# Performance work log

Measured on AMD Instinct MI355X. Metric: run time of the kernel, lower is better.

The kernel has to match this reference:

```python
import jax, jax.numpy as jnp
import numpy as np

B, T, U, H, M, K, C = 64, 800, 80, 512, 20, 10, 80  # batch, tsteps, char len, rnn_size, nmixtures, kmixtures, char_vec_len


def _lstm(x, W, Uw, b):
    """Keras-semantics LSTM (gate order i,f,g,o), zero initial state. x: [B,T,D] -> [B,T,H]."""
    xg = jnp.einsum('btd,dh->bth', x, W) + b  # precompute input contribution
    h0 = jnp.zeros((x.shape[0], Uw.shape[0]), x.dtype)
    c0 = jnp.zeros_like(h0)

    def step(carry, zt):
        h, c = carry
        z = zt + h @ Uw
        i, f, g, o = jnp.split(z, 4, axis=-1)
        c = jax.nn.sigmoid(f) * c + jax.nn.sigmoid(i) * jnp.tanh(g)
        h = jax.nn.sigmoid(o) * jnp.tanh(c)
        return (h, c), h

    _, hs = jax.lax.scan(step, (h0, c0), jnp.swapaxes(xg, 0, 1))
    return jnp.swapaxes(hs, 0, 1)


def _forward(stroke_data, char_seq, kappa0, W0, U0, b0, W1, U1, b1, W2, U2, b2, Wa, ba, Wm, bm):
    lstm0_out = _lstm(stroke_data, W0, U0, b0)  # [B,T,H]
    # Attention window: the per-timestep loop in the source only carries kappa,
    # which is a running sum of exp(kappa_offset) -> vectorize via cumsum.
    abk = jnp.exp(jnp.einsum('bth,hk->btk', lstm0_out, Wa) + ba)  # [B,T,3K]
    alpha, beta, koff = jnpp_split = jnp.split(abk, 3, axis=-1)
    kappa = kappa0[:, None, :, 0] + jnp.cumsum(koff, axis=1)  # [B,T,K]
    u = jnp.arange(char_seq.shape[1], dtype=stroke_data.dtype)  # [U]
    # phi: [B,T,U] = sum_k alpha * exp(-beta * (kappa - u)^2)
    phi = jnp.sum(alpha[..., None] * jnp.exp(-beta[..., None] * (kappa[..., None] - u) ** 2), axis=2)
    windows = jnp.einsum('btu,buc->btc', phi, char_seq)  # [B,T,C]
    aug = jnp.concatenate([lstm0_out, windows, stroke_data], axis=-1)
    lstm1_out = _lstm(aug, W1, U1, b1)
    lstm2_out = _lstm(lstm1_out, W2, U2, b2)
    mdn = jnp.einsum('bth,hn->btn', lstm2_out, Wm) + bm  # [B,T,1+6M]
    eos_hat = mdn[..., 0:1]
    pi_hat, mu1, mu2, s1_hat, s2_hat, rho_hat = jnp.split(mdn[..., 1:], 6, axis=-1)
    return jnp.concatenate([
        jax.nn.sigmoid(-eos_hat),
        jax.nn.softmax(pi_hat, axis=-1),
        mu1, mu2,
        jnp.exp(s1_hat), jnp.exp(s2_hat),
        jnp.tanh(rho_hat),
    ], axis=-1)  # [B,T,1+6M]


def setup_inputs() -> dict:
    key = jax.random.key(0)
    ks = jax.random.split(key, 12)
    init = lambda k, shape: jax.random.truncated_normal(k, -2.0, 2.0, shape, jnp.float32) * 0.075
    return {
        'stroke_data': jax.random.normal(ks[0], (B, T, 3), jnp.float32),
        'char_seq': jax.nn.one_hot(jax.random.randint(ks[1], (B, U), 0, C), C, dtype=jnp.float32),
        'kappa0': jnp.zeros((B, K, 1), jnp.float32),
        'W0': init(ks[2], (3, 4 * H)), 'U0': init(ks[3], (H, 4 * H)), 'b0': jnp.zeros((4 * H,)),
        'W1': init(ks[4], (H + C + 3, 4 * H)), 'U1': init(ks[5], (H, 4 * H)), 'b1': jnp.zeros((4 * H,)),
        'W2': init(ks[6], (H, 4 * H)), 'U2': init(ks[7], (H, 4 * H)), 'b2': jnp.zeros((4 * H,)),
        'Wa': init(ks[8], (H, 3 * K)),
        'ba': -3.0 + 0.25 * jax.random.truncated_normal(ks[9], -2.0, 2.0, (3 * K,), jnp.float32),
        'Wm': init(ks[10], (H, 1 + 6 * M)), 'bm': jnp.zeros((1 + 6 * M,)),
    }


def reference(stroke_data, char_seq, kappa0, W0, U0, b0, W1, U1, b1, W2, U2, b2, Wa, ba, Wm, bm):
    return _forward(stroke_data, char_seq, kappa0, W0, U0, b0, W1, U1, b1, W2, U2, b2, Wa, ba, Wm, bm)
```

## Files before the change

kernel.cpp:

```cpp
#include <hip/hip_runtime.h>

typedef unsigned short u16;
typedef unsigned int u32;
typedef short v8s __attribute__((ext_vector_type(8)));
typedef float v4f __attribute__((ext_vector_type(4)));
typedef unsigned int v4u __attribute__((ext_vector_type(4)));
typedef unsigned int v2u __attribute__((ext_vector_type(2)));

#define MFMA16 __builtin_amdgcn_mfma_f32_16x16x32_bf16

constexpr int TT = 800;
constexpr int NBLK = 178;

constexpr int AUGB  = 2240;
constexpr int AUG2B = 2048;

constexpr size_t AUGR_OFF  = 131072;
constexpr size_t AUG2R_OFF = AUGR_OFF + (size_t)4 * 64 * AUGB;
constexpr size_t WAT_OFF   = AUG2R_OFF + (size_t)4 * 64 * AUG2B;
constexpr size_t WS_ZERO   = WAT_OFF + (size_t)32 * 512 * 2;

constexpr u32 SMEM_BYTES = 82944;

enum { G_S0D = 0, G_SAD = 1, G_S1D = 2, G_S2D = 3, G_S1R = 4, G_SAR = 5, G_S2R = 6, G_SMR = 7 };

__device__ __forceinline__ float bf2f(u16 u) { return __uint_as_float(((u32)u) << 16); }
__device__ __forceinline__ u16 f2bf(float f) {
    u32 x = __float_as_uint(f);
    return (u16)((x + 0x7fffu + ((x >> 16) & 1u)) >> 16);
}
__device__ __forceinline__ short f2bfs(float f) { return (short)f2bf(f); }
__device__ __forceinline__ float sigf(float x) { return 1.f / (1.f + __expf(-x)); }
__device__ __forceinline__ float tanhf2(float x) { return 1.f - 2.f / (1.f + __expf(2.f * x)); }

__device__ __forceinline__ __amdgpu_buffer_rsrc_t mkrsrc(const void* p) {
    return __builtin_amdgcn_make_buffer_rsrc((void*)p, (short)0, -1, 0x00020000);
}
__device__ __forceinline__ v4u ldu4(__amdgpu_buffer_rsrc_t r, int off) {
    return __builtin_amdgcn_raw_buffer_load_b128(r, off, 0, 17);
}
__device__ __forceinline__ v2u ldu8(__amdgpu_buffer_rsrc_t r, int off) {
    return __builtin_amdgcn_raw_buffer_load_b64(r, off, 0, 17);
}
__device__ __forceinline__ void stq8(__amdgpu_buffer_rsrc_t r, int off, u16 a, u16 b, u16 c, u16 d) {
    v2u t; t[0] = (u32)a | ((u32)b << 16); t[1] = (u32)c | ((u32)d << 16);
    __builtin_amdgcn_raw_buffer_store_b64(t, r, off, 0, 17);
}
__device__ __forceinline__ void stq4(__amdgpu_buffer_rsrc_t r, int off, u16 a, u16 b) {
    u32 t = (u32)a | ((u32)b << 16);
    __builtin_amdgcn_raw_buffer_store_b32(t, r, off, 0, 17);
}

__device__ __forceinline__ void publish(u32* ctrl, int g, int t, int sub) {
    __hip_atomic_fetch_add(ctrl + g * 4096 + (t & 3) * 1024 + (sub & 15) * 64, 1u,
                           __ATOMIC_RELAXED, __HIP_MEMORY_SCOPE_AGENT);
}
__device__ __forceinline__ void wait4(u32* ctrl,
    int g0, int t0, u32 n0, int m0, int g1, int t1, u32 n1, int m1,
    int g2, int t2, u32 n2, int m2, int g3, int t3, u32 n3, int m3)
{
    if (threadIdx.x < 64) {
        const int lane = threadIdx.x;
        const int cl = lane >> 4, k = lane & 15;
        int g, tt, mb; u32 nn;
        if (cl == 0)      { g = g0; tt = t0; nn = n0; mb = m0; }
        else if (cl == 1) { g = g1; tt = t1; nn = n1; mb = m1; }
        else if (cl == 2) { g = g2; tt = t2; nn = n2; mb = m2; }
        else              { g = g3; tt = t3; nn = n3; mb = m3; }
        const u32 tgt = (g >= 0 && tt >= 0) ? nn * (u32)((tt >> 2) + 1) : 0u;
        u32* p = (tgt > 0) ? (ctrl + g * 4096 + (tt & 3) * 1024 + (mb + (k & 7)) * 64) : (u32*)0;
        int sp = 0;
        for (;;) {
            u32 v = p ? __hip_atomic_load(p, __ATOMIC_RELAXED, __HIP_MEMORY_SCOPE_AGENT) : 0u;
            v += __shfl_xor(v, 1); v += __shfl_xor(v, 2);
            v += __shfl_xor(v, 4); v += __shfl_xor(v, 8);
            const bool bad = (tgt > 0) && (v < tgt);
            if (__ballot(bad) == 0ull) break;
            if (sp >= 2) __builtin_amdgcn_s_sleep(4);
            else if (sp == 1) __builtin_amdgcn_s_sleep(1);
            sp++;
        }
    }
    __syncthreads();
}

__global__ void wat_init(const float* __restrict__ Wa, u16* __restrict__ WaT) {
    __amdgpu_buffer_rsrc_t r = mkrsrc(WaT);
    for (int idx = blockIdx.x * 256 + threadIdx.x; idx < 32 * 512 / 2; idx += gridDim.x * 256) {
        const int e0 = idx * 2, e1 = e0 + 1;
        const int n0 = e0 >> 9, k0 = e0 & 511;
        const int n1 = e1 >> 9, k1 = e1 & 511;
        const u16 a = (n0 < 30) ? f2bf(Wa[k0 * 30 + n0]) : (u16)0;
        const u16 b = (n1 < 30) ? f2bf(Wa[k1 * 30 + n1]) : (u16)0;
        stq4(r, idx * 4, a, b);
    }
}

__global__ __launch_bounds__(256, 1) void hw_main(
    const float* __restrict__ stroke, const float* __restrict__ charseq, const float* __restrict__ kappa0,
    const float* __restrict__ W0, const float* __restrict__ U0, const float* __restrict__ b0,
    const float* __restrict__ W1, const float* __restrict__ U1, const float* __restrict__ b1,
    const float* __restrict__ W2, const float* __restrict__ U2, const float* __restrict__ b2,
    const float* __restrict__ ba, const float* __restrict__ Wm, const float* __restrict__ bm,
    float* __restrict__ out, char* __restrict__ ws)
{
    extern __shared__ __align__(16) char smem[];
    u32* ctrl = (u32*)ws;
    u16* augr  = (u16*)(ws + AUGR_OFF);
    u16* aug2r = (u16*)(ws + AUG2R_OFF);
    const u16* WaT = (const u16*)(ws + WAT_OFF);

    const int blk = blockIdx.x, tid = threadIdx.x;
    const int wave = tid >> 6, lane = tid & 63;
    const int quad = lane >> 4, l15 = lane & 15;

    if (blk < 32) {
        const int cs = blk & 15, mg = blk >> 4;
        const int mb = mg * 8, sub = mb + (cs & 7);
        __amdgpu_buffer_rsrc_t ra = mkrsrc(augr);
        u16*   aL  = (u16*)smem;
        float* zb  = (float*)(smem + 33280);
        float* w0s = (float*)(smem + 50176);
        float* b0s = (float*)(smem + 51712);
        if (tid < 128) {
            const int cn2 = (tid >> 5) * 512 + cs * 32 + (tid & 31);
            b0s[tid] = b0[cn2];
            #pragma unroll
            for (int d = 0; d < 3; d++) w0s[d * 128 + tid] = W0[d * 2048 + cn2];
        }
        v8s bw0[16], bw1[16];
        {
            const int cnA = wave * 512 + cs * 32 + l15;
            const int cnB = cnA + 16;
            #pragma unroll
            for (int kc = 0; kc < 16; kc++)
                #pragma unroll
                for (int j = 0; j < 8; j++) {
                    const int k = kc * 32 + quad * 8 + j;
                    bw0[kc][j] = f2bfs(U0[k * 2048 + cnA]);
                    bw1[kc][j] = f2bfs(U0[k * 2048 + cnB]);
                }
        }
        float cst[4] = {0.f, 0.f, 0.f, 0.f};
        const int bl_ = tid & 31;
        const int bpre = mg * 32 + bl_;
        __syncthreads();
        #pragma unroll 1
        for (int t = 0; t < TT; t++) {
            const float xx0 = stroke[(bpre * TT + t) * 3 + 0];
            const float xx1 = stroke[(bpre * TT + t) * 3 + 1];
            const float xx2 = stroke[(bpre * TT + t) * 3 + 2];
            wait4(ctrl, G_S0D, t - 1, 32, mb, G_S1R, t - 4, 64, mb, G_SAR, t - 4, 16, mb, -1, 0, 0, 0);
            {
                const int base = (((t + 3) & 3) * 64 + mg * 32) * AUGB;
                #pragma unroll
                for (int c8 = 0; c8 < 8; c8++) {
                    const int c = tid + 256 * c8;
                    const int row = c >> 6, off = c & 63;
                    v4u d = ldu4(ra, base + row * AUGB + off * 16);
                    *(v4u*)((char*)aL + row * 1040 + off * 16) = d;
                }
            }
            __syncthreads();
            v4f c0a = {0,0,0,0}, c0b = {0,0,0,0}, c1a = {0,0,0,0}, c1b = {0,0,0,0};
            const int xo = quad * 16;
            #pragma unroll
            for (int kc = 0; kc < 16; kc++) {
                v8s x0 = *(const v8s*)((const char*)aL + l15 * 1040 + kc * 64 + xo);
                v8s x1 = *(const v8s*)((const char*)aL + (16 + l15) * 1040 + kc * 64 + xo);
                c0a = MFMA16(x0, bw0[kc], c0a, 0, 0, 0);
                c1a = MFMA16(x0, bw1[kc], c1a, 0, 0, 0);
                c0b = MFMA16(x1, bw0[kc], c0b, 0, 0, 0);
                c1b = MFMA16(x1, bw1[kc], c1b, 0, 0, 0);
            }
            const int n0 = wave * 32 + l15, n1 = n0 + 16;
            #pragma unroll
            for (int r = 0; r < 4; r++) {
                zb[(quad * 4 + r) * 132 + n0] = c0a[r];
                zb[(quad * 4 + r) * 132 + n1] = c1a[r];
                zb[(16 + quad * 4 + r) * 132 + n0] = c0b[r];
                zb[(16 + quad * 4 + r) * 132 + n1] = c1b[r];
            }
            __syncthreads();
            {
                const int bl = tid & 31, jj = tid >> 5;
                const int b = mg * 32 + bl;
                u16 hv[4];
                #pragma unroll
                for (int m = 0; m < 4; m++) {
                    const int j = jj * 4 + m;
                    float z[4];
                    #pragma unroll
                    for (int g = 0; g < 4; g++) {
                        const int n = g * 32 + j;
                        z[g] = zb[bl * 132 + n] + b0s[n] + xx0 * w0s[n] + xx1 * w0s[128 + n] + xx2 * w0s[256 + n];
                    }
                    const float cc = sigf(z[1]) * cst[m] + sigf(z[0]) * tanhf2(z[2]);
                    cst[m] = cc;
                    hv[m] = f2bf(sigf(z[3]) * tanhf2(cc));
                }
                stq8(ra, ((t & 3) * 64 + b) * AUGB + (cs * 32 + jj * 4) * 2, hv[0], hv[1], hv[2], hv[3]);
            }
            __syncthreads();
            if (tid == 0) publish(ctrl, G_S0D, t, sub);
        }
    } else if (blk < 96) {
        const int q = blk - 32, cs = q >> 1, mg = q & 1;
        const int mb = mg * 8, sub = mb + (cs & 7);
        __amdgpu_buffer_rsrc_t ra = mkrsrc(augr);
        __amdgpu_buffer_rsrc_t r2 = mkrsrc(aug2r);
        u16*   aL  = (u16*)smem;
        float* zb  = (float*)(smem + 72192);
        float* b1s = (float*)(smem + 80896);
        if (tid < 64) b1s[tid] = b1[(tid >> 4) * 512 + cs * 16 + (tid & 15)];
        v8s bw[35];
        {
            const int cn = wave * 512 + cs * 16 + l15;
            #pragma unroll
            for (int kc = 0; kc < 35; kc++)
                #pragma unroll
                for (int j = 0; j < 8; j++) {
                    const int k = kc * 32 + quad * 8 + j;
                    short v = 0;
                    if (k < 595) v = f2bfs(W1[k * 2048 + cn]);
                    else if (k >= 596 && k < 1108) v = f2bfs(U1[(k - 596) * 2048 + cn]);
                    bw[kc][j] = v;
                }
        }
        if (tid < 32) { v4u z4 = {0,0,0,0}; *(v4u*)((char*)aL + tid * 2256 + 2224) = z4; }
        float cst[2] = {0.f, 0.f};
        __syncthreads();
        #pragma unroll 1
        for (int t = 0; t < TT; t++) {
            wait4(ctrl, G_S0D, t, 32, mb, G_SAD, t, 16, mb, G_S2R, t - 4, 64, mb, -1, 0, 0, 0);
            {
                const int base = ((t & 3) * 64 + mg * 32) * AUGB;
                #pragma unroll
                for (int c10 = 0; c10 < 10; c10++) {
                    const int c = tid + 256 * c10;
                    if (c < 2400) {
                        const int row = c / 75, off = c - row * 75;
                        v4u d = ldu4(ra, base + row * AUGB + off * 16);
                        *(v4u*)((char*)aL + row * 2256 + off * 16) = d;
                    }
                }
            }
            __syncthreads();
            if (tid == 0) publish(ctrl, G_S1R, t, sub);
            wait4(ctrl, G_S1D, t - 1, 64, mb, -1, 0, 0, 0, -1, 0, 0, 0, -1, 0, 0, 0);
            {
                const int base = ((t & 3) * 64 + mg * 32) * AUGB;
                if (tid < 32) {
                    v2u d8 = ldu8(ra, base + tid * AUGB + 1192);
                    *(v2u*)((char*)aL + tid * 2256 + 1192) = d8;
                }
                #pragma unroll
                for (int c8 = 0; c8 < 8; c8++) {
                    const int c = tid + 256 * c8;
                    const int row = c >> 6, off = 75 + (c & 63);
                    v4u d = ldu4(ra, base + row * AUGB + off * 16);
                    *(v4u*)((char*)aL + row * 2256 + off * 16) = d;
                }
            }
            v4f c0 = {0,0,0,0}, c1 = {0,0,0,0};
            const int xo = quad * 16;
            #pragma unroll
            for (int kc = 0; kc < 18; kc++) {
                v8s x0 = *(const v8s*)((const char*)aL + l15 * 2256 + kc * 64 + xo);
                v8s x1 = *(const v8s*)((const char*)aL + (16 + l15) * 2256 + kc * 64 + xo);
                c0 = MFMA16(x0, bw[kc], c0, 0, 0, 0);
                c1 = MFMA16(x1, bw[kc], c1, 0, 0, 0);
            }
            __syncthreads();
            #pragma unroll
            for (int kc = 18; kc < 35; kc++) {
                v8s x0 = *(const v8s*)((const char*)aL + l15 * 2256 + kc * 64 + xo);
                v8s x1 = *(const v8s*)((const char*)aL + (16 + l15) * 2256 + kc * 64 + xo);
                c0 = MFMA16(x0, bw[kc], c0, 0, 0, 0);
                c1 = MFMA16(x1, bw[kc], c1, 0, 0, 0);
            }
            #pragma unroll
            for (int r = 0; r < 4; r++) {
                zb[(quad * 4 + r) * 68 + wave * 17 + l15] = c0[r];
                zb[(16 + quad * 4 + r) * 68 + wave * 17 + l15] = c1[r];
            }
            __syncthreads();
            {
                const int bl = tid & 31, jj = tid >> 5;
                const int b = mg * 32 + bl;
                u16 hv[2];
                #pragma unroll
                for (int m = 0; m < 2; m++) {
                    const int j = jj * 2 + m;
                    float z[4];
                    #pragma unroll
                    for (int g = 0; g < 4; g++)
                        z[g] = zb[bl * 68 + g * 17 + j] + b1s[g * 16 + j];
                    const float cc = sigf(z[1]) * cst[m] + sigf(z[0]) * tanhf2(z[2]);
                    cst[m] = cc;
                    hv[m] = f2bf(sigf(z[3]) * tanhf2(cc));
                }
                stq4(ra, (((t + 1) & 3) * 64 + b) * AUGB + (596 + cs * 16 + jj * 2) * 2, hv[0], hv[1]);
                stq4(r2, ((t & 3) * 64 + b) * AUG2B + (cs * 16 + jj * 2) * 2, hv[0], hv[1]);
            }
            __syncthreads();
            if (tid == 0) publish(ctrl, G_S1D, t, sub);
        }
    } else if (blk < 160) {
        const int q = blk - 96, cs = q >> 1, mg = q & 1;
        const int mb = mg * 8, sub = mb + (cs & 7);
        __amdgpu_buffer_rsrc_t r2 = mkrsrc(aug2r);
        u16*   aL  = (u16*)smem;
        float* zb  = (float*)(smem + 66048);
        float* b2s = (float*)(smem + 74752);
        if (tid < 64) b2s[tid] = b2[(tid >> 4) * 512 + cs * 16 + (tid & 15)];
        v8s bw[32];
        {
            const int cn = wave * 512 + cs * 16 + l15;
            #pragma unroll
            for (int kc = 0; kc < 32; kc++)
                #pragma unroll
                for (int j = 0; j < 8; j++) {
                    const int k = kc * 32 + quad * 8 + j;
                    bw[kc][j] = (k < 512) ? f2bfs(W2[k * 2048 + cn]) : f2bfs(U2[(k - 512) * 2048 + cn]);
                }
        }
        float cst[2] = {0.f, 0.f};
        __syncthreads();
        #pragma unroll 1
        for (int t = 0; t < TT; t++) {
            wait4(ctrl, G_S1D, t, 64, mb, G_SMR, t - 4, 2, mb, -1, 0, 0, 0, -1, 0, 0, 0);
            {
                const int base = ((t & 3) * 64 + mg * 32) * AUG2B;
                #pragma unroll
                for (int c8 = 0; c8 < 8; c8++) {
                    const int c = tid + 256 * c8;
                    const int row = c >> 6, off = c & 63;
                    v4u d = ldu4(r2, base + row * AUG2B + off * 16);
                    *(v4u*)((char*)aL + row * 2064 + off * 16) = d;
                }
            }
            __syncthreads();
            if (tid == 0) publish(ctrl, G_S2R, t, sub);
            wait4(ctrl, G_S2D, t - 1, 64, mb, -1, 0, 0, 0, -1, 0, 0, 0, -1, 0, 0, 0);
            {
                const int base = ((t & 3) * 64 + mg * 32) * AUG2B;
                #pragma unroll
                for (int c8 = 0; c8 < 8; c8++) {
                    const int c = tid + 256 * c8;
                    const int row = c >> 6, off = 64 + (c & 63);
                    v4u d = ldu4(r2, base + row * AUG2B + off * 16);
                    *(v4u*)((char*)aL + row * 2064 + off * 16) = d;
                }
            }
            v4f c0 = {0,0,0,0}, c1 = {0,0,0,0};
            const int xo = quad * 16;
            #pragma unroll
            for (int kc = 0; kc < 16; kc++) {
                v8s x0 = *(const v8s*)((const char*)aL + l15 * 2064 + kc * 64 + xo);
                v8s x1 = *(const v8s*)((const char*)aL + (16 + l15) * 2064 + kc * 64 + xo);
                c0 = MFMA16(x0, bw[kc], c0, 0, 0, 0);
                c1 = MFMA16(x1, bw[kc], c1, 0, 0, 0);
            }
            __syncthreads();
            #pragma unroll
            for (int kc = 16; kc < 32; kc++) {
                v8s x0 = *(const v8s*)((const char*)aL + l15 * 2064 + kc * 64 + xo);
                v8s x1 = *(const v8s*)((const char*)aL + (16 + l15) * 2064 + kc * 64 + xo);
                c0 = MFMA16(x0, bw[kc], c0, 0, 0, 0);
                c1 = MFMA16(x1, bw[kc], c1, 0, 0, 0);
            }
            #pragma unroll
            for (int r = 0; r < 4; r++) {
                zb[(quad * 4 + r) * 68 + wave * 17 + l15] = c0[r];
                zb[(16 + quad * 4 + r) * 68 + wave * 17 + l15] = c1[r];
            }
            __syncthreads();
            {
                const int bl = tid & 31, jj = tid >> 5;
                const int b = mg * 32 + bl;
                u16 hv[2];
                #pragma unroll
                for (int m = 0; m < 2; m++) {
                    const int j = jj * 2 + m;
                    float z[4];
                    #pragma unroll
                    for (int g = 0; g < 4; g++)
                        z[g] = zb[bl * 68 + g * 17 + j] + b2s[g * 16 + j];
                    const float cc = sigf(z[1]) * cst[m] + sigf(z[0]) * tanhf2(z[2]);
                    cst[m] = cc;
                    hv[m] = f2bf(sigf(z[3]) * tanhf2(cc));
                }
                stq4(r2, (((t + 1) & 3) * 64 + b) * AUG2B + (512 + cs * 16 + jj * 2) * 2, hv[0], hv[1]);
            }
            __syncthreads();
            if (tid == 0) publish(ctrl, G_S2D, t, sub);
        }
    } else if (blk < 176) {
        const int a = blk - 160;
        const int mg = a >> 3, mb = mg * 8, sub = mb + (a & 7);
        const int b = a * 4 + wave;
        __amdgpu_buffer_rsrc_t ra = mkrsrc(augr);
        u16*   watl = (u16*)smem;
        u16*   hrow = (u16*)(smem + 33280);
        float* phis = (float*)(smem + 37440);
        u16*   idxs = (u16*)(smem + 38720);
        {
            #pragma unroll
            for (int c8 = 0; c8 < 8; c8++) {
                const int c = tid + 256 * c8;
                const int row = c >> 6, off = c & 63;
                *(v4u*)((char*)watl + row * 1040 + off * 16) = *(const v4u*)(WaT + row * 512 + off * 8);
            }
        }
        #pragma unroll
        for (int rep = 0; rep < 2; rep++) {
            const int u = rep * 64 + lane;
            if (u < 80) {
                int c = 0;
                #pragma unroll 1
                for (int cc = 0; cc < 80; cc++)
                    if (charseq[b * 6400 + u * 80 + cc] > 0.5f) c = cc;
                idxs[wave * 80 + u] = (u16)c;
            }
        }
        float kap = (lane < 10) ? kappa0[b * 10 + lane] : 0.f;
        const float baf = (lane < 30) ? ba[lane] : 0.f;
        const int nn = lane & 31;
        const int k0 = (lane >> 5) * 256;
        const u16* wrow = watl + nn * 520 + k0;
        __syncthreads();
        #pragma unroll 1
        for (int t = 0; t < TT; t++) {
            float sx0 = 0.f, sx1 = 0.f;
            if (lane == 40) { sx0 = stroke[(b * TT + t) * 3 + 0]; sx1 = stroke[(b * TT + t) * 3 + 1]; }
            else if (lane == 41) { sx0 = stroke[(b * TT + t) * 3 + 2]; }
            wait4(ctrl, G_S0D, t, 32, mb, G_S1R, t - 4, 64, mb, -1, 0, 0, 0, -1, 0, 0, 0);
            {
                const int row = tid >> 6, off = tid & 63;
                v4u d = ldu4(ra, ((t & 3) * 64 + a * 4 + row) * AUGB + off * 16);
                *(v4u*)((char*)hrow + row * 1040 + off * 16) = d;
            }
            __syncthreads();
            if (tid == 0) publish(ctrl, G_SAR, t, sub);
            float acc = 0.f;
            #pragma unroll
            for (int kk = 0; kk < 32; kk++) {
                v8s hv = *(const v8s*)((const char*)hrow + wave * 1040 + (k0 + kk * 8) * 2);
                v8s wv = *(const v8s*)(wrow + kk * 8);
                #pragma unroll
                for (int e = 0; e < 8; e++) acc += bf2f((u16)hv[e]) * bf2f((u16)wv[e]);
            }
            acc += __shfl_xor(acc, 32);
            const float abk = __expf(acc + baf);
            const float kofv = __shfl(abk, 20 + (lane < 10 ? lane : 0));
            if (lane < 10) kap += kofv;
            const float u1f = (float)lane;
            float p1 = 0.f, p2 = 0.f;
            #pragma unroll
            for (int kk = 0; kk < 10; kk++) {
                const float al = __shfl(abk, kk);
                const float be = __shfl(abk, 10 + kk);
                const float kp = __shfl(kap, kk);
                const float d1 = kp - u1f, d2 = kp - (u1f + 64.f);
                p1 += al * __expf(-be * d1 * d1);
                p2 += al * __expf(-be * d2 * d2);
            }
            phis[wave * 80 + lane] = p1;
            if (lane < 16) phis[wave * 80 + 64 + lane] = p2;
            __syncthreads();
            const int db = (((t & 3) * 64 + b) * AUGB) + 512 * 2;
            if (lane < 40) {
                const int c0 = 2 * lane;
                float w0 = 0.f, w1 = 0.f;
                #pragma unroll 1
                for (int u = 0; u < 80; u++) {
                    const float pv = phis[wave * 80 + u];
                    const int ix = (int)idxs[wave * 80 + u];
                    w0 += (ix == c0)     ? pv : 0.f;
                    w1 += (ix == c0 + 1) ? pv : 0.f;
                }
                stq4(ra, db + c0 * 2, f2bf(w0), f2bf(w1));
            } else if (lane == 40) {
                stq4(ra, db + 80 * 2, f2bf(sx0), f2bf(sx1));
            } else if (lane == 41) {
                stq4(ra, db + 82 * 2, f2bf(sx0), (u16)0);
            }
            __syncthreads();
            if (tid == 0) publish(ctrl, G_SAD, t, sub);
        }
    } else {
        const int mgs = blk - 176;
        const int mb = mgs * 8, sub = mb;
        __amdgpu_buffer_rsrc_t r2 = mkrsrc(aug2r);
        u16*   aL = (u16*)smem;
        float* zb = (float*)(smem + 33280);
        v8s bw0[16], bw1[16];
        {
            const int nA = wave * 32 + l15, nB = nA + 16;
            #pragma unroll
            for (int kc = 0; kc < 16; kc++)
                #pragma unroll
                for (int j = 0; j < 8; j++) {
                    const int k = kc * 32 + quad * 8 + j;
                    bw0[kc][j] = (nA < 121) ? f2bfs(Wm[k * 121 + nA]) : (short)0;
                    bw1[kc][j] = (nB < 121) ? f2bfs(Wm[k * 121 + nB]) : (short)0;
                }
        }
        __syncthreads();
        #pragma unroll 1
        for (int t = 0; t < TT; t++) {
            wait4(ctrl, G_S2D, t, 64, mb, -1, 0, 0, 0, -1, 0, 0, 0, -1, 0, 0, 0);
            {
                const int base = (((t + 1) & 3) * 64 + mgs * 32) * AUG2B + 1024;
                #pragma unroll
                for (int c8 = 0; c8 < 8; c8++) {
                    const int c = tid + 256 * c8;
                    const int row = c >> 6, off = c & 63;
                    v4u d = ldu4(r2, base + row * AUG2B + off * 16);
                    *(v4u*)((char*)aL + row * 1040 + off * 16) = d;
                }
            }
            __syncthreads();
            if (tid == 0) publish(ctrl, G_SMR, t, sub);
            v4f c0a = {0,0,0,0}, c0b = {0,0,0,0}, c1a = {0,0,0,0}, c1b = {0,0,0,0};
            const int xo = quad * 16;
            #pragma unroll
            for (int kc = 0; kc < 16; kc++) {
                v8s x0 = *(const v8s*)((const char*)aL + l15 * 1040 + kc * 64 + xo);
                v8s x1 = *(const v8s*)((const char*)aL + (16 + l15) * 1040 + kc * 64 + xo);
                c0a = MFMA16(x0, bw0[kc], c0a, 0, 0, 0);
                c1a = MFMA16(x0, bw1[kc], c1a, 0, 0, 0);
                c0b = MFMA16(x1, bw0[kc], c0b, 0, 0, 0);
                c1b = MFMA16(x1, bw1[kc], c1b, 0, 0, 0);
            }
            const int n0 = wave * 32 + l15, n1 = n0 + 16;
            #pragma unroll
            for (int r = 0; r < 4; r++) {
                zb[(quad * 4 + r) * 132 + n0] = c0a[r];
                zb[(quad * 4 + r) * 132 + n1] = c1a[r];
                zb[(16 + quad * 4 + r) * 132 + n0] = c0b[r];
                zb[(16 + quad * 4 + r) * 132 + n1] = c1b[r];
            }
            __syncthreads();
            {
                const int b8 = tid >> 3, g8 = tid & 7;
                const int b = mgs * 32 + b8;
                const float* zr = zb + b8 * 132;
                float* orow = out + ((size_t)(b * TT + t)) * 121;
                if (g8 == 0) {
                    orow[0] = sigf(-(zr[0] + bm[0]));
                    float mx = -1e30f;
                    float zv[20];
                    #pragma unroll 1
                    for (int nl = 1; nl <= 20; nl++) { zv[nl - 1] = zr[nl] + bm[nl]; mx = fmaxf(mx, zv[nl - 1]); }
                    float ss = 0.f;
                    #pragma unroll 1
                    for (int nl = 0; nl < 20; nl++) { zv[nl] = __expf(zv[nl] - mx); ss += zv[nl]; }
                    const float inv = 1.f / ss;
                    #pragma unroll 1
                    for (int nl = 0; nl < 20; nl++) orow[nl + 1] = zv[nl] * inv;
                } else if (g8 <= 2) {
                    const int s0 = 21 + (g8 - 1) * 20;
                    #pragma unroll 1
                    for (int nl = s0; nl < s0 + 20; nl++) orow[nl] = zr[nl] + bm[nl];
                } else if (g8 <= 4) {
                    const int s0 = 61 + (g8 - 3) * 20;
                    #pragma unroll 1
                    for (int nl = s0; nl < s0 + 20; nl++) orow[nl] = __expf(zr[nl] + bm[nl]);
                } else if (g8 <= 6) {
                    const int s0 = 101 + (g8 - 5) * 10;
                    #pragma unroll 1
                    for (int nl = s0; nl < s0 + 10; nl++) orow[nl] = tanhf2(zr[nl] + bm[nl]);
                }
            }
            __syncthreads();
        }
    }
}

extern "C" void kernel_launch(void* const* d_in, const int* in_sizes, int n_in,
                              void* d_out, int out_size, void* d_ws, size_t ws_size,
                              hipStream_t stream) {
    const float* stroke  = (const float*)d_in[0];
    const float* charseq = (const float*)d_in[1];
    const float* kappa0  = (const float*)d_in[2];
    const float* W0 = (const float*)d_in[3];
    const float* U0 = (const float*)d_in[4];
    const float* b0 = (const float*)d_in[5];
    const float* W1 = (const float*)d_in[6];
    const float* U1 = (const float*)d_in[7];
    const float* b1 = (const float*)d_in[8];
    const float* W2 = (const float*)d_in[9];
    const float* U2 = (const float*)d_in[10];
    const float* b2 = (const float*)d_in[11];
    const float* Wa = (const float*)d_in[12];
    const float* ba = (const float*)d_in[13];
    const float* Wm = (const float*)d_in[14];
    const float* bm = (const float*)d_in[15];
    char* ws = (char*)d_ws;

    static bool attr_done = false;
    if (!attr_done) {
        hipFuncSetAttribute((const void*)hw_main,
                            hipFuncAttributeMaxDynamicSharedMemorySize, SMEM_BYTES);
        attr_done = true;
    }

    hipMemsetAsync(d_ws, 0, WS_ZERO, stream);
    wat_init<<<8, 256, 0, stream>>>(Wa, (u16*)(ws + WAT_OFF));
    hw_main<<<NBLK, 256, SMEM_BYTES, stream>>>(stroke, charseq, kappa0, W0, U0, b0,
                                               W1, U1, b1, W2, U2, b2, ba, Wm, bm,
                                               (float*)d_out, ws);
}
```

Measured before the change: 8.748 ms.

## Map pipeline stages to XCDs and use cache-local loads when co-located

The persistent kernel now launches 256 blocks and assigns stages by blockIdx modulo 8, so that each LSTM1/LSTM2 column group lands on a single XCD under round-robin dispatch. At startup, each group checks via HW_REG_XCC_ID whether all its blocks share one XCD. If they do, recurrent hidden-state exchanges use L2-coherent loads and stores (aux 1) instead of system-coherent ones, and stage 2 gets a private hidden-state buffer. The layer-1 input row is padded so the recurrent half is aligned, flag polling moves to inline-asm buffer loads, and the backoff sleep is shortened. The cost is many idle blocks and reliance on the dispatch-to-XCD mapping, with a fallback path if that mapping does not hold.

```diff
diff --git a/kernel.cpp b/kernel.cpp
--- a/kernel.cpp
+++ b/kernel.cpp
@@ -10,17 +10,18 @@
 #define MFMA16 __builtin_amdgcn_mfma_f32_16x16x32_bf16
 
 constexpr int TT = 800;
-constexpr int NBLK = 178;
-
-constexpr int AUGB  = 2240;
+constexpr int NBLK = 256;
+
+constexpr int AUGB  = 2304;
 constexpr int AUG2B = 2048;
 
 constexpr size_t AUGR_OFF  = 131072;
 constexpr size_t AUG2R_OFF = AUGR_OFF + (size_t)4 * 64 * AUGB;
 constexpr size_t WAT_OFF   = AUG2R_OFF + (size_t)4 * 64 * AUG2B;
-constexpr size_t WS_ZERO   = WAT_OFF + (size_t)32 * 512 * 2;
-
-constexpr u32 SMEM_BYTES = 82944;
+constexpr size_t S2P_OFF   = WAT_OFF + (size_t)32 * 512 * 2;
+constexpr size_t WS_ZERO   = S2P_OFF + (size_t)4 * 64 * 1024;
+
+constexpr u32 SMEM_BYTES = 83200;
 
 enum { G_S0D = 0, G_SAD = 1, G_S1D = 2, G_S2D = 3, G_S1R = 4, G_SAR = 5, G_S2R = 6, G_SMR = 7 };
 
@@ -36,19 +37,36 @@
 __device__ __forceinline__ __amdgpu_buffer_rsrc_t mkrsrc(const void* p) {
     return __builtin_amdgcn_make_buffer_rsrc((void*)p, (short)0, -1, 0x00020000);
 }
-__device__ __forceinline__ v4u ldu4(__amdgpu_buffer_rsrc_t r, int off) {
-    return __builtin_amdgcn_raw_buffer_load_b128(r, off, 0, 17);
-}
-__device__ __forceinline__ v2u ldu8(__amdgpu_buffer_rsrc_t r, int off) {
-    return __builtin_amdgcn_raw_buffer_load_b64(r, off, 0, 17);
-}
+template<int AUX>
+__device__ __forceinline__ v4u ldu4t(__amdgpu_buffer_rsrc_t r, int off) {
+    return __builtin_amdgcn_raw_buffer_load_b128(r, off, 0, AUX);
+}
+__device__ __forceinline__ v4u ldu4(__amdgpu_buffer_rsrc_t r, int off) { return ldu4t<17>(r, off); }
 __device__ __forceinline__ void stq8(__amdgpu_buffer_rsrc_t r, int off, u16 a, u16 b, u16 c, u16 d) {
     v2u t; t[0] = (u32)a | ((u32)b << 16); t[1] = (u32)c | ((u32)d << 16);
     __builtin_amdgcn_raw_buffer_store_b64(t, r, off, 0, 17);
 }
-__device__ __forceinline__ void stq4(__amdgpu_buffer_rsrc_t r, int off, u16 a, u16 b) {
+template<int AUX>
+__device__ __forceinline__ void stq4t(__amdgpu_buffer_rsrc_t r, int off, u16 a, u16 b) {
     u32 t = (u32)a | ((u32)b << 16);
-    __builtin_amdgcn_raw_buffer_store_b32(t, r, off, 0, 17);
+    __builtin_amdgcn_raw_buffer_store_b32(t, r, off, 0, AUX);
+}
+__device__ __forceinline__ void stq4(__amdgpu_buffer_rsrc_t r, int off, u16 a, u16 b) { stq4t<17>(r, off, a, b); }
+
+__device__ __forceinline__ v4u mksrd(const void* p) {
+    v4u r;
+    r[0] = (u32)(size_t)p;
+    r[1] = (u32)((size_t)p >> 32);
+    r[2] = 0xFFFFFFFFu;
+    r[3] = 0x00020000u;
+    return r;
+}
+__device__ __forceinline__ u32 poll_ld(v4u srd, int off) {
+    u32 v;
+    asm volatile("buffer_load_dword %0, %1, %2, 0 offen sc0 sc1\n\t"
+                 "s_waitcnt vmcnt(0)"
+                 : "=v"(v) : "v"(off), "s"(srd) : "memory");
+    return v;
 }
 
 __device__ __forceinline__ void publish(u32* ctrl, int g, int t, int sub) {
@@ -68,15 +86,16 @@
         else if (cl == 2) { g = g2; tt = t2; nn = n2; mb = m2; }
         else              { g = g3; tt = t3; nn = n3; mb = m3; }
         const u32 tgt = (g >= 0 && tt >= 0) ? nn * (u32)((tt >> 2) + 1) : 0u;
-        u32* p = (tgt > 0) ? (ctrl + g * 4096 + (tt & 3) * 1024 + (mb + (k & 7)) * 64) : (u32*)0;
+        const v4u srd = mksrd(ctrl);
+        const int boff = (g >= 0) ? (g * 4096 + ((tt & 3)) * 1024 + (mb + (k & 7)) * 64) * 4 : 0;
         int sp = 0;
         for (;;) {
-            u32 v = p ? __hip_atomic_load(p, __ATOMIC_RELAXED, __HIP_MEMORY_SCOPE_AGENT) : 0u;
+            u32 v = (tgt > 0) ? poll_ld(srd, boff) : 0u;
             v += __shfl_xor(v, 1); v += __shfl_xor(v, 2);
             v += __shfl_xor(v, 4); v += __shfl_xor(v, 8);
             const bool bad = (tgt > 0) && (v < tgt);
             if (__ballot(bad) == 0ull) break;
-            if (sp >= 2) __builtin_amdgcn_s_sleep(4);
+            if (sp >= 2) __builtin_amdgcn_s_sleep(2);
             else if (sp == 1) __builtin_amdgcn_s_sleep(1);
             sp++;
         }
@@ -108,15 +127,56 @@
     u32* ctrl = (u32*)ws;
     u16* augr  = (u16*)(ws + AUGR_OFF);
     u16* aug2r = (u16*)(ws + AUG2R_OFF);
+    u16* s2p   = (u16*)(ws + S2P_OFF);
     const u16* WaT = (const u16*)(ws + WAT_OFF);
 
-    const int blk = blockIdx.x, tid = threadIdx.x;
+    const int tid = threadIdx.x;
     const int wave = tid >> 6, lane = tid & 63;
     const int quad = lane >> 4, l15 = lane & 15;
 
-    if (blk < 32) {
-        const int cs = blk & 15, mg = blk >> 4;
-        const int mb = mg * 8, sub = mb + (cs & 7);
+    const int pb = blockIdx.x;
+    const int x = pb & 7, r = pb >> 3;
+    int stage = -1, cs = 0, mg = 0, aa = 0;
+    if (x == 0)      { stage = 1; mg = 0; cs = r; }
+    else if (x == 1) { stage = 1; mg = 1; cs = r; }
+    else if (x == 2) { stage = 2; mg = 0; cs = r; }
+    else if (x == 3) { stage = 2; mg = 1; cs = r; }
+    else if (x == 4 || x == 5) {
+        mg = x - 4;
+        if (r < 16)      { stage = 0; cs = r; }
+        else if (r < 24) { stage = 3; aa = mg * 8 + (r - 16); }
+        else if (r == 24){ stage = 4; }
+    }
+    if (stage < 0) return;
+    const int mb = mg * 8;
+
+    bool lok = false;
+    if (stage == 1 || stage == 2) {
+        __shared__ int lokf;
+        if (tid == 0) {
+            const int cg = (stage - 1) * 2 + mg;
+            u32 myx;
+            asm volatile("s_getreg_b32 %0, hwreg(HW_REG_XCC_ID)" : "=s"(myx));
+            u32* mp = ctrl + cg * 4096 + 32;
+            u32* cp = ctrl + cg * 4096 + 36;
+            __hip_atomic_fetch_or(mp, 1u << (myx & 31), __ATOMIC_RELAXED, __HIP_MEMORY_SCOPE_AGENT);
+            __hip_atomic_fetch_add(cp, 1u, __ATOMIC_RELEASE, __HIP_MEMORY_SCOPE_AGENT);
+            int sp = 0;
+            for (;;) {
+                u32 c = __hip_atomic_load(cp, __ATOMIC_ACQUIRE, __HIP_MEMORY_SCOPE_AGENT);
+                if (c >= 32u) break;
+                if (sp >= 2) __builtin_amdgcn_s_sleep(2);
+                else if (sp == 1) __builtin_amdgcn_s_sleep(1);
+                sp++;
+            }
+            u32 m = __hip_atomic_load(mp, __ATOMIC_ACQUIRE, __HIP_MEMORY_SCOPE_AGENT);
+            lokf = (__popc(m) == 1) ? 1 : 0;
+        }
+        __syncthreads();
+        lok = (lokf != 0);
+    }
+
+    if (stage == 0) {
         __amdgpu_buffer_rsrc_t ra = mkrsrc(augr);
         u16*   aL  = (u16*)smem;
         float* zb  = (float*)(smem + 33280);
@@ -142,8 +202,7 @@
                 }
         }
         float cst[4] = {0.f, 0.f, 0.f, 0.f};
-        const int bl_ = tid & 31;
-        const int bpre = mg * 32 + bl_;
+        const int bpre = mg * 32 + (tid & 31);
         __syncthreads();
         #pragma unroll 1
         for (int t = 0; t < TT; t++) {
@@ -175,11 +234,11 @@
             }
             const int n0 = wave * 32 + l15, n1 = n0 + 16;
             #pragma unroll
-            for (int r = 0; r < 4; r++) {
-                zb[(quad * 4 + r) * 132 + n0] = c0a[r];
-                zb[(quad * 4 + r) * 132 + n1] = c1a[r];
-                zb[(16 + quad * 4 + r) * 132 + n0] = c0b[r];
-                zb[(16 + quad * 4 + r) * 132 + n1] = c1b[r];
+            for (int rr = 0; rr < 4; rr++) {
+                zb[(quad * 4 + rr) * 132 + n0] = c0a[rr];
+                zb[(quad * 4 + rr) * 132 + n1] = c1a[rr];
+                zb[(16 + quad * 4 + rr) * 132 + n0] = c0b[rr];
+                zb[(16 + quad * 4 + rr) * 132 + n1] = c1b[rr];
             }
             __syncthreads();
             {
@@ -202,87 +261,92 @@
                 stq8(ra, ((t & 3) * 64 + b) * AUGB + (cs * 32 + jj * 4) * 2, hv[0], hv[1], hv[2], hv[3]);
             }
             __syncthreads();
-            if (tid == 0) publish(ctrl, G_S0D, t, sub);
-        }
-    } else if (blk < 96) {
-        const int q = blk - 32, cs = q >> 1, mg = q & 1;
-        const int mb = mg * 8, sub = mb + (cs & 7);
+            if (tid == 0) publish(ctrl, G_S0D, t, mb + (cs & 7));
+        }
+    } else if (stage == 1) {
         __amdgpu_buffer_rsrc_t ra = mkrsrc(augr);
         __amdgpu_buffer_rsrc_t r2 = mkrsrc(aug2r);
         u16*   aL  = (u16*)smem;
-        float* zb  = (float*)(smem + 72192);
-        float* b1s = (float*)(smem + 80896);
+        float* zb  = (float*)(smem + 74240);
+        float* b1s = (float*)(smem + 82944);
         if (tid < 64) b1s[tid] = b1[(tid >> 4) * 512 + cs * 16 + (tid & 15)];
-        v8s bw[35];
+        v8s bw[36];
         {
             const int cn = wave * 512 + cs * 16 + l15;
             #pragma unroll
-            for (int kc = 0; kc < 35; kc++)
+            for (int kc = 0; kc < 36; kc++)
                 #pragma unroll
                 for (int j = 0; j < 8; j++) {
                     const int k = kc * 32 + quad * 8 + j;
                     short v = 0;
                     if (k < 595) v = f2bfs(W1[k * 2048 + cn]);
-                    else if (k >= 596 && k < 1108) v = f2bfs(U1[(k - 596) * 2048 + cn]);
+                    else if (k >= 640 && k < 1152) v = f2bfs(U1[(k - 640) * 2048 + cn]);
                     bw[kc][j] = v;
                 }
         }
-        if (tid < 32) { v4u z4 = {0,0,0,0}; *(v4u*)((char*)aL + tid * 2256 + 2224) = z4; }
+        if (tid < 32) {
+            v4u z4 = {0,0,0,0};
+            #pragma unroll
+            for (int i = 0; i < 5; i++) *(v4u*)((char*)aL + tid * 2320 + 1200 + i * 16) = z4;
+        }
         float cst[2] = {0.f, 0.f};
         __syncthreads();
         #pragma unroll 1
         for (int t = 0; t < TT; t++) {
             wait4(ctrl, G_S0D, t, 32, mb, G_SAD, t, 16, mb, G_S2R, t - 4, 64, mb, -1, 0, 0, 0);
-            {
-                const int base = ((t & 3) * 64 + mg * 32) * AUGB;
+            const int base = ((t & 3) * 64 + mg * 32) * AUGB;
+            {
                 #pragma unroll
                 for (int c10 = 0; c10 < 10; c10++) {
                     const int c = tid + 256 * c10;
                     if (c < 2400) {
                         const int row = c / 75, off = c - row * 75;
                         v4u d = ldu4(ra, base + row * AUGB + off * 16);
-                        *(v4u*)((char*)aL + row * 2256 + off * 16) = d;
+                        *(v4u*)((char*)aL + row * 2320 + off * 16) = d;
                     }
                 }
             }
             __syncthreads();
-            if (tid == 0) publish(ctrl, G_S1R, t, sub);
+            if (tid == 0) publish(ctrl, G_S1R, t, mb + (cs & 7));
             wait4(ctrl, G_S1D, t - 1, 64, mb, -1, 0, 0, 0, -1, 0, 0, 0, -1, 0, 0, 0);
-            {
-                const int base = ((t & 3) * 64 + mg * 32) * AUGB;
-                if (tid < 32) {
-                    v2u d8 = ldu8(ra, base + tid * AUGB + 1192);
-                    *(v2u*)((char*)aL + tid * 2256 + 1192) = d8;
-                }
+            if (lok) {
                 #pragma unroll
                 for (int c8 = 0; c8 < 8; c8++) {
                     const int c = tid + 256 * c8;
-                    const int row = c >> 6, off = 75 + (c & 63);
-                    v4u d = ldu4(ra, base + row * AUGB + off * 16);
-                    *(v4u*)((char*)aL + row * 2256 + off * 16) = d;
+                    const int row = c >> 6, off = 80 + (c & 63);
+                    v4u d = ldu4t<1>(ra, base + row * AUGB + off * 16);
+                    *(v4u*)((char*)aL + row * 2320 + off * 16) = d;
+                }
+            } else {
+                #pragma unroll
+                for (int c8 = 0; c8 < 8; c8++) {
+                    const int c = tid + 256 * c8;
+                    const int row = c >> 6, off = 80 + (c & 63);
+                    v4u d = ldu4t<17>(ra, base + row * AUGB + off * 16);
+                    *(v4u*)((char*)aL + row * 2320 + off * 16) = d;
                 }
             }
             v4f c0 = {0,0,0,0}, c1 = {0,0,0,0};
             const int xo = quad * 16;
             #pragma unroll
-            for (int kc = 0; kc < 18; kc++) {
-                v8s x0 = *(const v8s*)((const char*)aL + l15 * 2256 + kc * 64 + xo);
-                v8s x1 = *(const v8s*)((const char*)aL + (16 + l15) * 2256 + kc * 64 + xo);
+            for (int kc = 0; kc < 19; kc++) {
+                v8s x0 = *(const v8s*)((const char*)aL + l15 * 2320 + kc * 64 + xo);
+                v8s x1 = *(const v8s*)((const char*)aL + (16 + l15) * 2320 + kc * 64 + xo);
                 c0 = MFMA16(x0, bw[kc], c0, 0, 0, 0);
                 c1 = MFMA16(x1, bw[kc], c1, 0, 0, 0);
             }
             __syncthreads();
             #pragma unroll
-            for (int kc = 18; kc < 35; kc++) {
-                v8s x0 = *(const v8s*)((const char*)aL + l15 * 2256 + kc * 64 + xo);
-                v8s x1 = *(const v8s*)((const char*)aL + (16 + l15) * 2256 + kc * 64 + xo);
+            for (int kc = 20; kc < 36; kc++) {
+                v8s x0 = *(const v8s*)((const char*)aL + l15 * 2320 + kc * 64 + xo);
+                v8s x1 = *(const v8s*)((const char*)aL + (16 + l15) * 2320 + kc * 64 + xo);
                 c0 = MFMA16(x0, bw[kc], c0, 0, 0, 0);
                 c1 = MFMA16(x1, bw[kc], c1, 0, 0, 0);
             }
             #pragma unroll
-            for (int r = 0; r < 4; r++) {
-                zb[(quad * 4 + r) * 68 + wave * 17 + l15] = c0[r];
-                zb[(16 + quad * 4 + r) * 68 + wave * 17 + l15] = c1[r];
+            for (int rr = 0; rr < 4; rr++) {
+                zb[(quad * 4 + rr) * 68 + wave * 17 + l15] = c0[rr];
+                zb[(16 + quad * 4 + rr) * 68 + wave * 17 + l15] = c1[rr];
             }
             __syncthreads();
             {
@@ -300,16 +364,17 @@
                     cst[m] = cc;
                     hv[m] = f2bf(sigf(z[3]) * tanhf2(cc));
                 }
-                stq4(ra, (((t + 1) & 3) * 64 + b) * AUGB + (596 + cs * 16 + jj * 2) * 2, hv[0], hv[1]);
+                const int hoff = (((t + 1) & 3) * 64 + b) * AUGB + (640 + cs * 16 + jj * 2) * 2;
+                if (lok) stq4t<1>(ra, hoff, hv[0], hv[1]);
+                else     stq4t<17>(ra, hoff, hv[0], hv[1]);
                 stq4(r2, ((t & 3) * 64 + b) * AUG2B + (cs * 16 + jj * 2) * 2, hv[0], hv[1]);
             }
             __syncthreads();
-            if (tid == 0) publish(ctrl, G_S1D, t, sub);
-        }
-    } else if (blk < 160) {
-        const int q = blk - 96, cs = q >> 1, mg = q & 1;
-        const int mb = mg * 8, sub = mb + (cs & 7);
-        __amdgpu_buffer_rsrc_t r2 = mkrsrc(aug2r);
+            if (tid == 0) publish(ctrl, G_S1D, t, mb + (cs & 7));
+        }
+    } else if (stage == 2) {
+        __amdgpu_buffer_rsrc_t r2  = mkrsrc(aug2r);
+        __amdgpu_buffer_rsrc_t rp  = mkrsrc(s2p);
         u16*   aL  = (u16*)smem;
         float* zb  = (float*)(smem + 66048);
         float* b2s = (float*)(smem + 74752);
@@ -341,16 +406,25 @@
                 }
             }
             __syncthreads();
-            if (tid == 0) publish(ctrl, G_S2R, t, sub);
+            if (tid == 0) publish(ctrl, G_S2R, t, mb + (cs & 7));
             wait4(ctrl, G_S2D, t - 1, 64, mb, -1, 0, 0, 0, -1, 0, 0, 0, -1, 0, 0, 0);
-            {
-                const int base = ((t & 3) * 64 + mg * 32) * AUG2B;
+            if (lok) {
+                const int bp = ((t & 3) * 64 + mg * 32) * 1024;
                 #pragma unroll
                 for (int c8 = 0; c8 < 8; c8++) {
                     const int c = tid + 256 * c8;
-                    const int row = c >> 6, off = 64 + (c & 63);
-                    v4u d = ldu4(r2, base + row * AUG2B + off * 16);
-                    *(v4u*)((char*)aL + row * 2064 + off * 16) = d;
+                    const int row = c >> 6, off = c & 63;
+                    v4u d = ldu4t<1>(rp, bp + row * 1024 + off * 16);
+                    *(v4u*)((char*)aL + row * 2064 + (64 + off) * 16) = d;
+                }
+            } else {
+                const int base = ((t & 3) * 64 + mg * 32) * AUG2B;
+                #pragma unroll
+                for (int c8 = 0; c8 < 8; c8++) {
+                    const int c = tid + 256 * c8;
+                    const int row = c >> 6, off = c & 63;
+                    v4u d = ldu4t<17>(r2, base + row * AUG2B + (64 + off) * 16);
+                    *(v4u*)((char*)aL + row * 2064 + (64 + off) * 16) = d;
                 }
             }
             v4f c0 = {0,0,0,0}, c1 = {0,0,0,0};
@@ -371,9 +445,9 @@
                 c1 = MFMA16(x1, bw[kc], c1, 0, 0, 0);
             }
             #pragma unroll
-            for (int r = 0; r < 4; r++) {
-                zb[(quad * 4 + r) * 68 + wave * 17 + l15] = c0[r];
-                zb[(16 + quad * 4 + r) * 68 + wave * 17 + l15] = c1[r];
+            for (int rr = 0; rr < 4; rr++) {
+                zb[(quad * 4 + rr) * 68 + wave * 17 + l15] = c0[rr];
+                zb[(16 + quad * 4 + rr) * 68 + wave * 17 + l15] = c1[rr];
             }
             __syncthreads();
             {
@@ -392,13 +466,13 @@
                     hv[m] = f2bf(sigf(z[3]) * tanhf2(cc));
                 }
                 stq4(r2, (((t + 1) & 3) * 64 + b) * AUG2B + (512 + cs * 16 + jj * 2) * 2, hv[0], hv[1]);
-            }
-            __syncthreads();
-            if (tid == 0) publish(ctrl, G_S2D, t, sub);
-        }
-    } else if (blk < 176) {
-        const int a = blk - 160;
-        const int mg = a >> 3, mb = mg * 8, sub = mb + (a & 7);
+                if (lok) stq4t<1>(rp, (((t + 1) & 3) * 64 + b) * 1024 + (cs * 16 + jj * 2) * 2, hv[0], hv[1]);
+            }
+            __syncthreads();
+            if (tid == 0) publish(ctrl, G_S2D, t, mb + (cs & 7));
+        }
+    } else if (stage == 3) {
+        const int a = aa;
         const int b = a * 4 + wave;
         __amdgpu_buffer_rsrc_t ra = mkrsrc(augr);
         u16*   watl = (u16*)smem;
@@ -442,7 +516,7 @@
                 *(v4u*)((char*)hrow + row * 1040 + off * 16) = d;
             }
             __syncthreads();
-            if (tid == 0) publish(ctrl, G_SAR, t, sub);
+            if (tid == 0) publish(ctrl, G_SAR, t, mb + (a & 7));
             float acc = 0.f;
             #pragma unroll
             for (int kk = 0; kk < 32; kk++) {
@@ -487,11 +561,10 @@
                 stq4(ra, db + 82 * 2, f2bf(sx0), (u16)0);
             }
             __syncthreads();
-            if (tid == 0) publish(ctrl, G_SAD, t, sub);
+            if (tid == 0) publish(ctrl, G_SAD, t, mb + (a & 7));
         }
     } else {
-        const int mgs = blk - 176;
-        const int mb = mgs * 8, sub = mb;
+        const int mgs = mg;
         __amdgpu_buffer_rsrc_t r2 = mkrsrc(aug2r);
         u16*   aL = (u16*)smem;
         float* zb = (float*)(smem + 33280);
@@ -522,7 +595,7 @@
                 }
             }
             __syncthreads();
-            if (tid == 0) publish(ctrl, G_SMR, t, sub);
+            if (tid == 0) publish(ctrl, G_SMR, t, mb);
             v4f c0a = {0,0,0,0}, c0b = {0,0,0,0}, c1a = {0,0,0,0}, c1b = {0,0,0,0};
             const int xo = quad * 16;
             #pragma unroll
@@ -536,11 +609,11 @@
             }
             const int n0 = wave * 32 + l15, n1 = n0 + 16;
             #pragma unroll
-            for (int r = 0; r < 4; r++) {
-                zb[(quad * 4 + r) * 132 + n0] = c0a[r];
-                zb[(quad * 4 + r) * 132 + n1] = c1a[r];
-                zb[(16 + quad * 4 + r) * 132 + n0] = c0b[r];
-                zb[(16 + quad * 4 + r) * 132 + n1] = c1b[r];
+            for (int rr = 0; rr < 4; rr++) {
+                zb[(quad * 4 + rr) * 132 + n0] = c0a[rr];
+                zb[(quad * 4 + rr) * 132 + n1] = c1a[rr];
+                zb[(16 + quad * 4 + rr) * 132 + n0] = c0b[rr];
+                zb[(16 + quad * 4 + rr) * 132 + n1] = c1b[rr];
             }
             __syncthreads();
             {
```

New measurement: 9.010 ms. 1.03x slower.
